# Performance work log

Hardware: AMD Instinct MI355X
Metric: run time of the kernel (lower is better)

Reference implementation:

```python
import jax, jax.numpy as jnp
import numpy as np

W = 0.3  # recursive filter weight (thre in original code)


def setup_inputs() -> dict:
    key = jax.random.key(0)
    # [B, C, N, H, W]; recurrence runs along axis 2 (N frames)
    x = jax.random.normal(key, (4, 3, 32, 256, 256), dtype=jnp.float32)
    return {"x": x}


def reference(x):
    # y[0] = x[0]; y[i] = W * x[i] + (1 - W) * y[i-1]  along axis 2
    xs = jnp.moveaxis(x, 2, 0)  # [N, B, C, H, W] so scan runs over leading axis
    y0 = xs[0]

    def step(carry, xi):
        y = W * xi + (1.0 - W) * carry
        return y, y

    _, ys = jax.lax.scan(step, y0, xs[1:])
    out = jnp.concatenate([y0[None], ys], axis=0)  # [N, B, C, H, W]
    return jnp.moveaxis(out, 0, 2)  # back to [B, C, N, H, W]
```

## Files before the change

kernel.cpp:

```cpp
#include <hip/hip_runtime.h>


constexpr int   BC   = 4 * 3;
constexpr int   NFR  = 32;
constexpr int   HW4  = (256 * 256) / 4;
constexpr float WF   = 0.3f;
constexpr float OMW  = 1.0f - WF;

__global__ __launch_bounds__(256) void recfilt_kernel(const float4* __restrict__ x,
                                                      float4* __restrict__ y) {
    const int p  = blockIdx.x * blockDim.x + threadIdx.x;
    const int bc = p >> 14;
    const int hw = p & (HW4 - 1);
    const long base = (long)bc * NFR * HW4 + hw;

    float4 acc = x[base];
    y[base] = acc;
#pragma unroll
    for (int n = 1; n < NFR; ++n) {
        const long idx = base + (long)n * HW4;
        float4 xv = x[idx];
        acc.x = WF * xv.x + OMW * acc.x;
        acc.y = WF * xv.y + OMW * acc.y;
        acc.z = WF * xv.z + OMW * acc.z;
        acc.w = WF * xv.w + OMW * acc.w;
        y[idx] = acc;
    }
}

extern "C" void kernel_launch(void* const* d_in, const int* in_sizes, int n_in,
                              void* d_out, int out_size, void* d_ws, size_t ws_size,
                              hipStream_t stream) {
    const float4* x = (const float4*)d_in[0];
    float4*       y = (float4*)d_out;
    const int chains = BC * HW4;
    const int block  = 256;
    const int grid   = chains / block;
    recfilt_kernel<<<grid, block, 0, stream>>>(x, y);
}
```

Baseline: 178.7 us.

## Split each temporal recurrence into four segments combined via shared-memory carry

Each chain of 32 frames is now split into four 8-frame segments handled by different threads of the same block. Each segment runs a local scan from a zero start, publishes its last value to shared memory, then adds a carry built from the earlier segments, scaled by precomputed powers of 0.7. This gives four times as many threads and independent loads in flight, targeting the low occupancy and latency-bound memory access of the serial version. In exchange it adds a barrier, a little shared memory and extra FMAs, and the reassociated arithmetic can change rounding slightly.

```diff
diff --git a/kernel.cpp b/kernel.cpp
--- a/kernel.cpp
+++ b/kernel.cpp
@@ -1,31 +1,85 @@
 #include <hip/hip_runtime.h>
 
 
-constexpr int   BC   = 4 * 3;
-constexpr int   NFR  = 32;
-constexpr int   HW4  = (256 * 256) / 4;
-constexpr float WF   = 0.3f;
-constexpr float OMW  = 1.0f - WF;
+constexpr int   NFR = 32;
+constexpr int   HW4 = (256 * 256) / 4;
+constexpr int   FPS = 8;
+constexpr int   CPB = 64;
+constexpr float WF  = 0.3f;
+constexpr float OMW = 0.7f;
+
+constexpr float P1  = 0.7f;
+constexpr float P2  = P1 * 0.7f;
+constexpr float P3  = P2 * 0.7f;
+constexpr float P4  = P3 * 0.7f;
+constexpr float P5  = P4 * 0.7f;
+constexpr float P6  = P5 * 0.7f;
+constexpr float P7  = P6 * 0.7f;
+constexpr float P8  = P7 * 0.7f;
+constexpr float P16 = P8 * P8;
 
 __global__ __launch_bounds__(256) void recfilt_kernel(const float4* __restrict__ x,
                                                       float4* __restrict__ y) {
-    const int p  = blockIdx.x * blockDim.x + threadIdx.x;
-    const int bc = p >> 14;
-    const int hw = p & (HW4 - 1);
-    const long base = (long)bc * NFR * HW4 + hw;
+    const int tid = threadIdx.x;
+    const int c   = tid & (CPB - 1);
+    const int seg = tid >> 6;
+    const int q   = blockIdx.x * CPB + c;
+    const int bc  = q >> 14;
+    const int hw  = q & (HW4 - 1);
+    const long base = (long)bc * (NFR * HW4) + (long)seg * (FPS * HW4) + hw;
 
-    float4 acc = x[base];
-    y[base] = acc;
-#pragma unroll
-    for (int n = 1; n < NFR; ++n) {
-        const long idx = base + (long)n * HW4;
-        float4 xv = x[idx];
-        acc.x = WF * xv.x + OMW * acc.x;
-        acc.y = WF * xv.y + OMW * acc.y;
-        acc.z = WF * xv.z + OMW * acc.z;
-        acc.w = WF * xv.w + OMW * acc.w;
-        y[idx] = acc;
+    float4 v0 = x[base + 0 * HW4];
+    float4 v1 = x[base + 1 * HW4];
+    float4 v2 = x[base + 2 * HW4];
+    float4 v3 = x[base + 3 * HW4];
+    float4 v4 = x[base + 4 * HW4];
+    float4 v5 = x[base + 5 * HW4];
+    float4 v6 = x[base + 6 * HW4];
+    float4 v7 = x[base + 7 * HW4];
+
+    if (seg != 0) {
+        v0.x *= WF; v0.y *= WF; v0.z *= WF; v0.w *= WF;
     }
+#define STEP(a, b)                                      \
+    b.x = WF * b.x + OMW * a.x; b.y = WF * b.y + OMW * a.y; \
+    b.z = WF * b.z + OMW * a.z; b.w = WF * b.w + OMW * a.w;
+    STEP(v0, v1) STEP(v1, v2) STEP(v2, v3) STEP(v3, v4)
+    STEP(v4, v5) STEP(v5, v6) STEP(v6, v7)
+#undef STEP
+
+    __shared__ float4 lend[3][CPB];
+    if (seg < 3) lend[seg][c] = v7;
+    __syncthreads();
+
+    float4 carry = make_float4(0.f, 0.f, 0.f, 0.f);
+    if (seg == 1) {
+        carry = lend[0][c];
+    } else if (seg == 2) {
+        const float4 e0 = lend[0][c], e1 = lend[1][c];
+        carry.x = fmaf(P8, e0.x, e1.x);
+        carry.y = fmaf(P8, e0.y, e1.y);
+        carry.z = fmaf(P8, e0.z, e1.z);
+        carry.w = fmaf(P8, e0.w, e1.w);
+    } else if (seg == 3) {
+        const float4 e0 = lend[0][c], e1 = lend[1][c], e2 = lend[2][c];
+        carry.x = fmaf(P16, e0.x, fmaf(P8, e1.x, e2.x));
+        carry.y = fmaf(P16, e0.y, fmaf(P8, e1.y, e2.y));
+        carry.z = fmaf(P16, e0.z, fmaf(P8, e1.z, e2.z));
+        carry.w = fmaf(P16, e0.w, fmaf(P8, e1.w, e2.w));
+    }
+
+#define OUT(n, v, pk)                                   \
+    {                                                   \
+        float4 o;                                       \
+        o.x = fmaf(pk, carry.x, v.x);                   \
+        o.y = fmaf(pk, carry.y, v.y);                   \
+        o.z = fmaf(pk, carry.z, v.z);                   \
+        o.w = fmaf(pk, carry.w, v.w);                   \
+        y[base + n * HW4] = o;                          \
+    }
+    OUT(0, v0, P1) OUT(1, v1, P2) OUT(2, v2, P3) OUT(3, v3, P4)
+    OUT(4, v4, P5) OUT(5, v5, P6) OUT(6, v6, P7) OUT(7, v7, P8)
+#undef OUT
 }
 
 extern "C" void kernel_launch(void* const* d_in, const int* in_sizes, int n_in,
@@ -33,8 +87,7 @@
                               hipStream_t stream) {
     const float4* x = (const float4*)d_in[0];
     float4*       y = (float4*)d_out;
-    const int chains = BC * HW4;
-    const int block  = 256;
-    const int grid   = chains / block;
-    recfilt_kernel<<<grid, block, 0, stream>>>(x, y);
+    const int chains = 12 * HW4;
+    const int grid   = chains / CPB;
+    recfilt_kernel<<<grid, 256, 0, stream>>>(x, y);
 }
```

Result: no change. 175.3 us (-1.9%).
